# Performance work log

Measured on AMD Instinct MI355X. Metric: run time of the kernel, lower is better.

The kernel has to match this reference:

```python
import jax, jax.numpy as jnp
import numpy as np

NB_LABELS = 64
BOS = 61
EOS = 62
PAD = 63


def setup_inputs() -> dict:
    key = jax.random.key(0)
    k1, k2, k3 = jax.random.split(key, 3)
    B, S, L = 512, 1024, NB_LABELS
    emissions = jax.random.normal(k1, (B, S, L), dtype=jnp.float32)
    tags = jax.random.randint(k2, (B, S), 0, 61)  # avoid BOS/EOS/PAD ids
    mask = jnp.ones((B, S), dtype=jnp.float32)
    # transitions initialized as in CRF.init_weights()
    trans = jax.random.uniform(k3, (L, L), jnp.float32, -0.1, 0.1)
    trans = trans.at[:, BOS].set(-10000.0)
    trans = trans.at[EOS, :].set(-10000.0)
    trans = trans.at[PAD, :].set(-10000.0)
    trans = trans.at[:, PAD].set(-10000.0)
    trans = trans.at[PAD, EOS].set(0.0)
    trans = trans.at[PAD, PAD].set(0.0)
    return {"emissions": emissions, "transitions": trans, "tags": tags, "mask": mask}


def _gold_scores(emissions, transitions, tags, mask):
    # fully vectorized version of _compute_scores (no time loop needed)
    first_tags = tags[:, 0]
    last_idx = mask.astype(jnp.int32).sum(1) - 1  # (B,)
    last_tags = jnp.take_along_axis(tags, last_idx[:, None], axis=1)[:, 0]
    scores = transitions[BOS, first_tags]
    scores = scores + jnp.take_along_axis(emissions[:, 0], first_tags[:, None], axis=1)[:, 0]
    e = jnp.take_along_axis(emissions[:, 1:], tags[:, 1:, None], axis=2)[:, :, 0]  # (B,S-1)
    t = transitions[tags[:, :-1], tags[:, 1:]]  # (B,S-1)
    scores = scores + ((e + t) * mask[:, 1:]).sum(axis=1)
    scores = scores + transitions[last_tags, EOS]
    return scores


def _log_partition(emissions, transitions, mask):
    # forward algorithm via lax.scan; state alphas: (B, L)
    alpha0 = transitions[BOS][None, :] + emissions[:, 0]

    def step(alphas, xs):
        em_t, m_t = xs  # (B, L), (B,)
        # scores[b, prev, cur] = alphas[b, prev] + transitions[prev, cur] + em_t[b, cur]
        new = jax.nn.logsumexp(alphas[:, :, None] + transitions[None, :, :] + em_t[:, None, :], axis=1)
        alphas = m_t[:, None] * new + (1.0 - m_t[:, None]) * alphas
        return alphas, None

    xs = (jnp.swapaxes(emissions[:, 1:], 0, 1), jnp.swapaxes(mask[:, 1:], 0, 1))
    alphas, _ = jax.lax.scan(step, alpha0, xs)
    return jax.nn.logsumexp(alphas + transitions[:, EOS][None, :], axis=1)


def reference(emissions, transitions, tags, mask):
    scores = _gold_scores(emissions, transitions, tags, mask)
    partition = _log_partition(emissions, transitions, mask)
    # forward() returns the negative log-likelihood per batch element
    return partition - scores
```

## Files before the change

### kernel.cpp

```cpp
#include <hip/hip_runtime.h>
#include <hip/hip_bf16.h>

#define CRF_B 512
#define CRF_S 1024
#define CRF_L 64
#define CRF_BOS 61
#define CRF_EOS 62
#define CRF_NC 32
#define CRF_CK (CRF_S / CRF_NC)
#define CRF_W 8
#define GRP 16

typedef __attribute__((ext_vector_type(8))) short short8;
typedef __attribute__((ext_vector_type(4))) float f32x4;
#define UNR _Pragma("unroll")

__device__ __forceinline__ unsigned short f2bf(float x) {
    union { __hip_bfloat16 h; unsigned short u; } cv;
    cv.h = __float2bfloat16(x);
    return cv.u;
}

__global__ __launch_bounds__(64) void crf_gold_kernel(
    const float* __restrict__ em, const float* __restrict__ trans,
    const int* __restrict__ tags, const float* __restrict__ mask,
    float* __restrict__ gold)
{
    const int b = blockIdx.x;
    const int l = threadIdx.x;
    const float* emb = em + (size_t)b * CRF_S * CRF_L;
    const int*   tg  = tags + (size_t)b * CRF_S;
    const float* mk  = mask + (size_t)b * CRF_S;

    float acc = 0.f, msum = 0.f;
    for (int t = l; t < CRF_S; t += 64) {
        float m = mk[t];
        msum += m;
        if (t >= 1) {
            int ct = tg[t];
            int pt = tg[t - 1];
            acc += (emb[(size_t)t * CRF_L + ct] + trans[pt * CRF_L + ct]) * m;
        }
    }
    UNR
    for (int off = 32; off; off >>= 1) {
        acc  += __shfl_xor(acc, off);
        msum += __shfl_xor(msum, off);
    }
    if (l == 0) {
        int t0 = tg[0];
        acc += trans[CRF_BOS * CRF_L + t0] + emb[t0];
        int last = (int)(msum + 0.5f) - 1;
        int lt = tg[last];
        acc += trans[lt * CRF_L + CRF_EOS];
        gold[b] = acc;
    }
}


#define STEP(T, eeU, eeV, rawU, rawV, mU, mV)                                   \
  {                                                                             \
    short8 Bf0, Bf1;                                                            \
    UNR for (int e = 0; e < 8; ++e) {                                           \
        Bf0[e] = (short)f2bf(val[e >> 2][e & 3]);                               \
        Bf1[e] = (short)f2bf(val[2 + (e >> 2)][e & 3]);                         \
    }                                                                           \
    UNR for (int mt = 0; mt < 4; ++mt) {                                        \
        f32x4 acc = {0.f, 0.f, 0.f, 0.f};                                       \
        acc = __builtin_amdgcn_mfma_f32_16x16x32_bf16(Af[mt][0], Bf0, acc, 0, 0, 0); \
        acc = __builtin_amdgcn_mfma_f32_16x16x32_bf16(Af[mt][1], Bf1, acc, 0, 0, 0); \
        UNR for (int r = 0; r < 4; ++r) {                                       \
            float nv = acc[r] * eeU[mt * 4 + r];                                \
            val[mt][r] = (mU > 0.5f) ? nv : val[mt][r];                         \
        }                                                                       \
    }                                                                           \
    UNR for (int i = 0; i < 16; ++i) eeV[i] = __expf(rawV[i]);                  \
    { int tl = (T) + 2; if (tl > CRF_S - 1) tl = CRF_S - 1;                     \
      mU = mrow[tl <= te ? tl : te];                                            \
      UNR for (int mt = 0; mt < 4; ++mt) {                                      \
          f32x4 rv = *(const f32x4*)(erow + (size_t)tl * CRF_L + mt * 16);      \
          UNR for (int r = 0; r < 4; ++r) rawU[mt * 4 + r] = rv[r];             \
      } }                                                                       \
    if (((T) & 7) == 0) {                                                       \
        float rsc = __shfl(val[0][0], l & 15);                                  \
        Clog += __logf(rsc);                                                    \
        float inv = 1.0f / rsc;                                                 \
        UNR for (int mt = 0; mt < 4; ++mt)                                      \
            UNR for (int r = 0; r < 4; ++r) val[mt][r] *= inv;                  \
    }                                                                           \
    if ((T) == t_mid) a0 = Clog + __logf(__shfl(val[0][0], l & 15));            \
  }

__global__ __launch_bounds__(64) void crf_part_mfma(
    const float* __restrict__ em, const float* __restrict__ trans,
    const float* __restrict__ mask, float* __restrict__ G)
{
    const int c   = blockIdx.x & (CRF_NC - 1);
    const int grp = blockIdx.x / CRF_NC;
    const int l   = threadIdx.x;
    const int lj  = l & 15;
    const int g   = l >> 4;

    short8 Af[4][2];
    UNR for (int mt = 0; mt < 4; ++mt)
      UNR for (int kc = 0; kc < 2; ++kc) {
        short8 f;
        UNR for (int e = 0; e < 8; ++e) {
            int L = kc * 32 + (e >> 2) * 16 + g * 4 + (e & 3);
            f[e] = (short)f2bf(__expf(trans[L * CRF_L + mt * 16 + lj]));
        }
        Af[mt][kc] = f;
      }

    const int b = grp * GRP + lj;
    const float* erow = em + (size_t)b * (CRF_S * CRF_L) + g * 4;
    const float* mrow = mask + (size_t)b * CRF_S;

    const int t_mid = CRF_CK * c;
    int t1, te;
    float val[4][4];
    if (c == 0) {
        t1 = 1; te = CRF_CK;
        UNR for (int mt = 0; mt < 4; ++mt)
          UNR for (int r = 0; r < 4; ++r) {
            int n = mt * 16 + g * 4 + r;
            val[mt][r] = __expf(trans[CRF_BOS * CRF_L + n] + erow[mt * 16 + r]);
          }
    } else {
        t1 = t_mid - CRF_W + 1;
        te = (c == CRF_NC - 1) ? (CRF_S - 1) : (t_mid + CRF_CK);
        UNR for (int mt = 0; mt < 4; ++mt)
          UNR for (int r = 0; r < 4; ++r) val[mt][r] = 1.0f;
    }

    float Clog = 0.f, a0 = 0.f;

    float eeX[16], eeY[16], rawX[16], rawY[16], mX, mY;
    mX = mrow[t1];
    mY = mrow[t1 + 1];
    UNR for (int mt = 0; mt < 4; ++mt) {
        f32x4 r0 = *(const f32x4*)(erow + (size_t)t1 * CRF_L + mt * 16);
        f32x4 r1 = *(const f32x4*)(erow + (size_t)(t1 + 1) * CRF_L + mt * 16);
        UNR for (int r = 0; r < 4; ++r) {
            rawX[mt * 4 + r] = r0[r];
            rawY[mt * 4 + r] = r1[r];
        }
    }
    UNR for (int i = 0; i < 16; ++i) eeX[i] = __expf(rawX[i]);

    int t = t1;
    for (; t + 1 <= te; t += 2) {
        STEP(t,     eeX, eeY, rawX, rawY, mX, mY);
        STEP(t + 1, eeY, eeX, rawY, rawX, mY, mX);
    }
    if (t <= te) STEP(t, eeX, eeY, rawX, rawY, mX, mY);

    float a1;
    if (c == CRF_NC - 1) {
        float s = 0.f;
        UNR for (int mt = 0; mt < 4; ++mt)
          UNR for (int r = 0; r < 4; ++r)
            s += val[mt][r] * __expf(trans[(mt * 16 + g * 4 + r) * CRF_L + CRF_EOS]);
        s += __shfl_xor(s, 16);
        s += __shfl_xor(s, 32);
        a1 = Clog + __logf(s);
    } else {
        a1 = Clog + __logf(__shfl(val[0][0], l & 15));
    }
    if (l < 16) G[b * CRF_NC + c] = a1 - a0;
}

__global__ __launch_bounds__(256) void crf_combine(
    const float* __restrict__ G, const float* __restrict__ gold,
    float* __restrict__ out)
{
    int b = blockIdx.x * blockDim.x + threadIdx.x;
    if (b < CRF_B) {
        float s = 0.f;
        UNR for (int c = 0; c < CRF_NC; ++c) s += G[b * CRF_NC + c];
        out[b] = s - gold[b];
    }
}

extern "C" void kernel_launch(void* const* d_in, const int* in_sizes, int n_in,
                              void* d_out, int out_size, void* d_ws, size_t ws_size,
                              hipStream_t stream) {
    const float* em    = (const float*)d_in[0];
    const float* trans = (const float*)d_in[1];
    const int*   tags  = (const int*)d_in[2];
    const float* mask  = (const float*)d_in[3];
    float* out  = (float*)d_out;
    float* gold = (float*)d_ws;
    float* G    = (float*)d_ws + CRF_B;

    crf_part_mfma<<<(CRF_B / GRP) * CRF_NC, 64, 0, stream>>>(em, trans, mask, G);
    crf_gold_kernel<<<CRF_B, 64, 0, stream>>>(em, trans, tags, mask, gold);
    crf_combine<<<2, 256, 0, stream>>>(G, gold, out);
}
```

Baseline: 50.53 us.

## Fuse gold and partition kernels, double chunk count, deepen emission prefetch

Merges the gold-score and partition kernels into one launch, so gold blocks run alongside the partition blocks and one launch is removed. The sequence is split into 64 chunks instead of 32, each with a shorter warm-up window (6 instead of 8), which raises parallelism and shortens each serial chain. The emission prefetch is now three steps ahead instead of two, to hide global-load latency. Shorter chunks and a smaller warm-up window mean more redundant warm-up work in total, and they depend on the rescaled forward vectors converging within fewer steps.

```diff
diff --git a/kernel.cpp b/kernel.cpp
--- a/kernel.cpp
+++ b/kernel.cpp
@@ -6,10 +6,11 @@
 #define CRF_L 64
 #define CRF_BOS 61
 #define CRF_EOS 62
-#define CRF_NC 32
+#define CRF_NC 64
 #define CRF_CK (CRF_S / CRF_NC)
-#define CRF_W 8
+#define CRF_W 6
 #define GRP 16
+#define PART_BLOCKS ((CRF_B / GRP) * CRF_NC)
 
 typedef __attribute__((ext_vector_type(8))) short short8;
 typedef __attribute__((ext_vector_type(4))) float f32x4;
@@ -21,13 +22,12 @@
     return cv.u;
 }
 
-__global__ __launch_bounds__(64) void crf_gold_kernel(
+__device__ __forceinline__ void gold_body(
+    int b, int l,
     const float* __restrict__ em, const float* __restrict__ trans,
     const int* __restrict__ tags, const float* __restrict__ mask,
     float* __restrict__ gold)
 {
-    const int b = blockIdx.x;
-    const int l = threadIdx.x;
     const float* emb = em + (size_t)b * CRF_S * CRF_L;
     const int*   tg  = tags + (size_t)b * CRF_S;
     const float* mk  = mask + (size_t)b * CRF_S;
@@ -58,7 +58,7 @@
 }
 
 
-#define STEP(T, eeU, eeV, rawU, rawV, mU, mV)                                   \
+#define STEP(T, eeU, eeV, rawU, mU)                                             \
   {                                                                             \
     short8 Bf0, Bf1;                                                            \
     UNR for (int e = 0; e < 8; ++e) {                                           \
@@ -74,9 +74,12 @@
             val[mt][r] = (mU > 0.5f) ? nv : val[mt][r];                         \
         }                                                                       \
     }                                                                           \
-    UNR for (int i = 0; i < 16; ++i) eeV[i] = __expf(rawV[i]);                  \
-    { int tl = (T) + 2; if (tl > CRF_S - 1) tl = CRF_S - 1;                     \
-      mU = mrow[tl <= te ? tl : te];                                            \
+                          \
+    UNR for (int i = 0; i < 16; ++i) eeV[i] = __expf(rawU[i]);                  \
+                       \
+    { int tl = (T) + 3; if (tl > CRF_S - 1) tl = CRF_S - 1;                     \
+      int tm = (T) + 2; if (tm > te) tm = te;                                   \
+      mU = mrow[tm];                                                            \
       UNR for (int mt = 0; mt < 4; ++mt) {                                      \
           f32x4 rv = *(const f32x4*)(erow + (size_t)tl * CRF_L + mt * 16);      \
           UNR for (int r = 0; r < 4; ++r) rawU[mt * 4 + r] = rv[r];             \
@@ -91,13 +94,13 @@
     if ((T) == t_mid) a0 = Clog + __logf(__shfl(val[0][0], l & 15));            \
   }
 
-__global__ __launch_bounds__(64) void crf_part_mfma(
+__device__ __forceinline__ void part_body(
+    int pb, int l,
     const float* __restrict__ em, const float* __restrict__ trans,
     const float* __restrict__ mask, float* __restrict__ G)
 {
-    const int c   = blockIdx.x & (CRF_NC - 1);
-    const int grp = blockIdx.x / CRF_NC;
-    const int l   = threadIdx.x;
+    const int c   = pb & (CRF_NC - 1);
+    const int grp = pb / CRF_NC;
     const int lj  = l & 15;
     const int g   = l >> 4;
 
@@ -137,23 +140,26 @@
 
     float eeX[16], eeY[16], rawX[16], rawY[16], mX, mY;
     mX = mrow[t1];
-    mY = mrow[t1 + 1];
+    { int tn = t1 + 1; if (tn > te) tn = te; mY = mrow[tn]; }
     UNR for (int mt = 0; mt < 4; ++mt) {
         f32x4 r0 = *(const f32x4*)(erow + (size_t)t1 * CRF_L + mt * 16);
-        f32x4 r1 = *(const f32x4*)(erow + (size_t)(t1 + 1) * CRF_L + mt * 16);
+        int ta = t1 + 1; if (ta > CRF_S - 1) ta = CRF_S - 1;
+        int tb = t1 + 2; if (tb > CRF_S - 1) tb = CRF_S - 1;
+        f32x4 r1 = *(const f32x4*)(erow + (size_t)ta * CRF_L + mt * 16);
+        f32x4 r2 = *(const f32x4*)(erow + (size_t)tb * CRF_L + mt * 16);
         UNR for (int r = 0; r < 4; ++r) {
-            rawX[mt * 4 + r] = r0[r];
-            rawY[mt * 4 + r] = r1[r];
+            eeX[mt * 4 + r]  = __expf(r0[r]);
+            rawX[mt * 4 + r] = r1[r];
+            rawY[mt * 4 + r] = r2[r];
         }
     }
-    UNR for (int i = 0; i < 16; ++i) eeX[i] = __expf(rawX[i]);
 
     int t = t1;
     for (; t + 1 <= te; t += 2) {
-        STEP(t,     eeX, eeY, rawX, rawY, mX, mY);
-        STEP(t + 1, eeY, eeX, rawY, rawX, mY, mX);
-    }
-    if (t <= te) STEP(t, eeX, eeY, rawX, rawY, mX, mY);
+        STEP(t,     eeX, eeY, rawX, mX);
+        STEP(t + 1, eeY, eeX, rawY, mY);
+    }
+    if (t <= te) STEP(t, eeX, eeY, rawX, mX);
 
     float a1;
     if (c == CRF_NC - 1) {
@@ -170,6 +176,20 @@
     if (l < 16) G[b * CRF_NC + c] = a1 - a0;
 }
 
+__global__ __launch_bounds__(64) void crf_fused(
+    const float* __restrict__ em, const float* __restrict__ trans,
+    const int* __restrict__ tags, const float* __restrict__ mask,
+    float* __restrict__ gold, float* __restrict__ G)
+{
+    const int bid = blockIdx.x;
+    const int l   = threadIdx.x;
+    if (bid < CRF_B) {
+        gold_body(bid, l, em, trans, tags, mask, gold);
+    } else {
+        part_body(bid - CRF_B, l, em, trans, mask, G);
+    }
+}
+
 __global__ __launch_bounds__(256) void crf_combine(
     const float* __restrict__ G, const float* __restrict__ gold,
     float* __restrict__ out)
@@ -193,7 +213,6 @@
     float* gold = (float*)d_ws;
     float* G    = (float*)d_ws + CRF_B;
 
-    crf_part_mfma<<<(CRF_B / GRP) * CRF_NC, 64, 0, stream>>>(em, trans, mask, G);
-    crf_gold_kernel<<<CRF_B, 64, 0, stream>>>(em, trans, tags, mask, gold);
+    crf_fused<<<CRF_B + PART_BLOCKS, 64, 0, stream>>>(em, trans, tags, mask, gold, G);
     crf_combine<<<2, 256, 0, stream>>>(G, gold, out);
 }
```

Measured after the change: 49.57 us. About the same (-1.9%).
